# Optimization experiments

Measured on AMD Instinct MI355X. Metric: run time of the kernel, lower is better.

Reference implementation:

```python
import jax, jax.numpy as jnp
import numpy as np

N_NODES = 50000
N_EDGES = 640000
IN_DIM = 5
HID = 128
NUM_GRAPHS = 512


def _graph_conv(x, src, dst, W_rel, b_rel, W_root):
    # PyG GraphConv (aggr='add'): out = lin_rel(sum_{j in N(i)} x_j) + lin_root(x_i)
    agg = jax.ops.segment_sum(x[src], dst, num_segments=N_NODES)  # [N, d_in]
    return agg @ W_rel + b_rel + x @ W_root


def setup_inputs() -> dict:
    key = jax.random.key(0)
    ks = jax.random.split(key, 16)
    x = jax.random.normal(ks[0], (N_NODES, IN_DIM), dtype=jnp.float32)
    edge_index = jax.random.randint(ks[1], (2, N_EDGES), 0, N_NODES, dtype=jnp.int32)
    batch = jnp.sort(jax.random.randint(ks[2], (N_NODES,), 0, NUM_GRAPHS, dtype=jnp.int32))

    def lin_w(k, fan_in, fan_out):
        bound = 1.0 / np.sqrt(fan_in)
        return jax.random.uniform(k, (fan_in, fan_out), jnp.float32, -bound, bound)

    def lin_b(k, fan_in, fan_out):
        bound = 1.0 / np.sqrt(fan_in)
        return jax.random.uniform(k, (fan_out,), jnp.float32, -bound, bound)

    params = {}
    dims = [(IN_DIM, HID), (HID, HID), (HID, HID)]
    for i, (di, do) in enumerate(dims):
        params[f"W_rel{i}"] = lin_w(ks[3 + 3 * i], di, do)
        params[f"b_rel{i}"] = lin_b(ks[4 + 3 * i], di, do)
        params[f"W_root{i}"] = lin_w(ks[5 + 3 * i], di, do)
    params["W_lin"] = lin_w(ks[12], HID, 1)
    params["b_lin"] = lin_b(ks[13], HID, 1)
    return {"x": x, "edge_index": edge_index, "batch": batch, **params}


def reference(x, edge_index, batch,
              W_rel0, b_rel0, W_root0,
              W_rel1, b_rel1, W_root1,
              W_rel2, b_rel2, W_root2,
              W_lin, b_lin):
    src, dst = edge_index[0], edge_index[1]
    # convs[:-1] with ReLU
    h = jax.nn.relu(_graph_conv(x, src, dst, W_rel0, b_rel0, W_root0))
    h = jax.nn.relu(_graph_conv(h, src, dst, W_rel1, b_rel1, W_root1))
    # last conv, no activation
    h = _graph_conv(h, src, dst, W_rel2, b_rel2, W_root2)
    # global_mean_pool over batch ids
    sums = jax.ops.segment_sum(h, batch, num_segments=NUM_GRAPHS)  # [G, HID]
    cnts = jax.ops.segment_sum(jnp.ones((h.shape[0],), h.dtype), batch, num_segments=NUM_GRAPHS)
    pooled = sums / jnp.maximum(cnts, 1.0)[:, None]
    # dropout(p=0.01) is identity in eval mode
    logits = pooled @ W_lin + b_lin  # [G, 1]
    return jax.nn.sigmoid(logits)
```

## Files before the change

kernel.cpp:

```cpp
#include <hip/hip_runtime.h>
#include <hip/hip_bf16.h>
#include <math.h>

#define N_NODES 50000
#define N_EDGES 640000
#define IN_DIM 5
#define HID 128
#define NGRAPH 512
#define BUCKET 64
#define GEMM_NBLK ((N_NODES + 63) / 64)
#define EDGE_BLK (N_EDGES / 1024)
#define TPREP_BLK 32
#define NROW_BLK ((N_NODES + 255) / 256)

typedef unsigned short u16;
typedef __attribute__((ext_vector_type(8))) short bf16x8;
typedef __attribute__((ext_vector_type(8))) unsigned short u16x8;
typedef __attribute__((ext_vector_type(4))) float f32x4;
typedef __attribute__((ext_vector_type(8))) float f32x8;
typedef __attribute__((ext_vector_type(4), aligned(4))) float f32x4u;

__device__ __forceinline__ float bf2f(u16 u) {
  union { unsigned int i; float f; } v; v.i = ((unsigned int)u) << 16; return v.f;
}
__device__ __forceinline__ u16 f2bf(float f) {
  return __bfloat16_as_ushort(__float2bfloat16(f));
}

__global__ __launch_bounds__(256) void setup_k(const int* __restrict__ src,
                                               const int* __restrict__ dst,
                                               int* __restrict__ cnt,
                                               int* __restrict__ slot,
                                               const float* __restrict__ W1rel,
                                               const float* __restrict__ W1root,
                                               u16* __restrict__ T1rel, u16* __restrict__ T1root,
                                               const float* __restrict__ Wrel2,
                                               const float* __restrict__ Wroot2,
                                               const float* __restrict__ b2,
                                               const float* __restrict__ Wlin,
                                               float* __restrict__ wvecs,
                                               const int* __restrict__ batch,
                                               int* __restrict__ nrow) {
  int b = blockIdx.x;
  if (b < EDGE_BLK) {
    int e0 = (b * 256 + threadIdx.x) * 4;
    int4 s4 = *(const int4*)(src + e0);
    int4 d4 = *(const int4*)(dst + e0);
    int ss[4] = {s4.x, s4.y, s4.z, s4.w};
    int dd[4] = {d4.x, d4.y, d4.z, d4.w};
#pragma unroll
    for (int j = 0; j < 4; ++j) {
      int pos = atomicAdd(&cnt[dd[j]], 1);
      if (pos < BUCKET) slot[(size_t)dd[j] * BUCKET + pos] = ss[j];
    }
  } else if (b < EDGE_BLK + TPREP_BLK) {
    int idx4 = ((b - EDGE_BLK) * 256 + threadIdx.x) * 4;
    int which = idx4 >> 14;
    int i = idx4 & (HID * HID - 1);
    const float* W = which == 0 ? W1rel : W1root;
    u16* T = which == 0 ? T1rel : T1root;
    int k = i >> 7, n = i & 127;
    float4 w4 = *(const float4*)(W + i);
    T[(n + 0) * HID + k] = f2bf(w4.x);
    T[(n + 1) * HID + k] = f2bf(w4.y);
    T[(n + 2) * HID + k] = f2bf(w4.z);
    T[(n + 3) * HID + k] = f2bf(w4.w);
  } else if (b == EDGE_BLK + TPREP_BLK) {
    int t = threadIdx.x;
    if (t < 128) {
      float s = 0.f;
      for (int c = 0; c < HID; ++c) s = fmaf(Wrel2[t * HID + c], Wlin[c], s);
      wvecs[t] = s;
    } else {
      int k = t - 128;
      float s = 0.f;
      for (int c = 0; c < HID; ++c) s = fmaf(Wroot2[k * HID + c], Wlin[c], s);
      wvecs[128 + k] = s;
    }
    if (t == 0) {
      float s = 0.f;
      for (int c = 0; c < HID; ++c) s = fmaf(b2[c], Wlin[c], s);
      wvecs[256] = s;
    }
  } else {
    int n = (b - EDGE_BLK - TPREP_BLK - 1) * 256 + threadIdx.x;
    if (n < N_NODES) {
      int bg = batch[n];
      int bp = (n == 0) ? -1 : batch[n - 1];
      for (int g = bp + 1; g <= bg; ++g) nrow[g] = n;
      if (n == N_NODES - 1) {
        for (int g = bg + 1; g <= NGRAPH; ++g) nrow[g] = N_NODES;
      }
    }
  }
}

__global__ __launch_bounds__(256, 3) void proj_gemm_k(const float* __restrict__ x,
                                                      const int* __restrict__ cnt,
                                                      const int* __restrict__ slot,
                                                      const float* __restrict__ Wrel0,
                                                      const float* __restrict__ Wroot0,
                                                      const float* __restrict__ brel0,
                                                      const u16* __restrict__ WrelT,
                                                      const u16* __restrict__ WrootT,
                                                      const float* __restrict__ bias1,
                                                      u16* __restrict__ Z,
                                                      u16* __restrict__ R) {
  __shared__ u16 As[64][136];
  __shared__ float A5s[64][IN_DIM];
  const int tid = threadIdx.x;
  const int r0 = blockIdx.x * 64;

  {
    const int li = tid >> 2;
    const int l4 = tid & 3;
    const int node = r0 + li;
    float a[IN_DIM];
#pragma unroll
    for (int k = 0; k < IN_DIM; ++k) a[k] = 0.f;
    if (node < N_NODES) {
      int deg = min(cnt[node], BUCKET);
      size_t base = (size_t)node * BUCKET;
      for (int j = l4; j < deg; j += 4) {
        int s = slot[base + j];
        f32x4u xv = *(const f32x4u*)(x + (size_t)s * IN_DIM);
        float x4 = x[(size_t)s * IN_DIM + 4];
#pragma unroll
        for (int k = 0; k < 4; ++k) a[k] += xv[k];
        a[4] += x4;
      }
    }
#pragma unroll
    for (int k = 0; k < IN_DIM; ++k) {
      a[k] += __shfl_xor(a[k], 1, 64);
      a[k] += __shfl_xor(a[k], 2, 64);
    }
    if (l4 == 0) {
#pragma unroll
      for (int k = 0; k < IN_DIM; ++k) A5s[li][k] = a[k];
    }
  }
  __syncthreads();

  {
    const int c0 = (tid & 63) * 2;
    const int rg = tid >> 6;
    float wr0[IN_DIM], wr1[IN_DIM], wo0[IN_DIM], wo1[IN_DIM];
#pragma unroll
    for (int k = 0; k < IN_DIM; ++k) {
      wr0[k] = Wrel0[k * HID + c0];
      wr1[k] = Wrel0[k * HID + c0 + 1];
      wo0[k] = Wroot0[k * HID + c0];
      wo1[k] = Wroot0[k * HID + c0 + 1];
    }
    const float b0 = brel0[c0], b1 = brel0[c0 + 1];
#pragma unroll
    for (int i = 0; i < 16; ++i) {
      int row = rg * 16 + i;
      int grow = r0 + row;
      float v0 = 0.f, v1 = 0.f;
      if (grow < N_NODES) {
        v0 = b0; v1 = b1;
        f32x4u xv = *(const f32x4u*)(x + (size_t)grow * IN_DIM);
        float x4 = x[(size_t)grow * IN_DIM + 4];
        float xr[IN_DIM] = {xv[0], xv[1], xv[2], xv[3], x4};
#pragma unroll
        for (int k = 0; k < IN_DIM; ++k) {
          float a = A5s[row][k];
          v0 = fmaf(a, wr0[k], fmaf(xr[k], wo0[k], v0));
          v1 = fmaf(a, wr1[k], fmaf(xr[k], wo1[k], v1));
        }
      }
      ushort2 w2;
      w2.x = f2bf(fmaxf(v0, 0.f));
      w2.y = f2bf(fmaxf(v1, 0.f));
      *(ushort2*)&As[row][c0] = w2;
    }
  }
  __syncthreads();

  const int wv = tid >> 6, lane = tid & 63;
  const int m = lane & 15, quad = lane >> 4;
  const u16* WT = (wv < 2) ? WrelT : WrootT;
  const int n0 = (wv & 1) * 64;

  f32x4 acc[4][4];
#pragma unroll
  for (int mt = 0; mt < 4; ++mt)
#pragma unroll
    for (int nt = 0; nt < 4; ++nt) acc[mt][nt] = (f32x4){0.f, 0.f, 0.f, 0.f};

#pragma unroll
  for (int ks = 0; ks < 4; ++ks) {
    int kb = ks * 32;
    bf16x8 af[4], bf[4];
#pragma unroll
    for (int mt = 0; mt < 4; ++mt)
      af[mt] = *(const bf16x8*)&As[mt * 16 + m][kb + quad * 8];
#pragma unroll
    for (int nt = 0; nt < 4; ++nt)
      bf[nt] = *(const bf16x8*)(WT + (size_t)(n0 + nt * 16 + m) * HID + kb + quad * 8);
#pragma unroll
    for (int mt = 0; mt < 4; ++mt)
#pragma unroll
      for (int nt = 0; nt < 4; ++nt)
        acc[mt][nt] = __builtin_amdgcn_mfma_f32_16x16x32_bf16(af[mt], bf[nt], acc[mt][nt], 0, 0, 0);
  }

  if (wv < 2) {
#pragma unroll
    for (int mt = 0; mt < 4; ++mt)
#pragma unroll
      for (int nt = 0; nt < 4; ++nt) {
        int col = n0 + nt * 16 + m;
#pragma unroll
        for (int r = 0; r < 4; ++r) {
          int row = r0 + mt * 16 + quad * 4 + r;
          if (row < N_NODES) Z[(size_t)row * HID + col] = f2bf(acc[mt][nt][r]);
        }
      }
  } else {
    float bl[4];
#pragma unroll
    for (int nt = 0; nt < 4; ++nt) bl[nt] = bias1[n0 + nt * 16 + m];
#pragma unroll
    for (int mt = 0; mt < 4; ++mt)
#pragma unroll
      for (int nt = 0; nt < 4; ++nt) {
        int col = n0 + nt * 16 + m;
#pragma unroll
        for (int r = 0; r < 4; ++r) {
          int row = r0 + mt * 16 + quad * 4 + r;
          if (row < N_NODES) R[(size_t)row * HID + col] = f2bf(acc[mt][nt][r] + bl[nt]);
        }
      }
  }
}

__device__ __forceinline__ void gather_node(const u16* __restrict__ Z,
                                            const int* __restrict__ esrc,
                                            int beg, int end, int q, int f8,
                                            f32x8& out) {
  f32x8 a0, a1;
#pragma unroll
  for (int j = 0; j < 8; ++j) { a0[j] = 0.f; a1[j] = 0.f; }
  int e = beg + q;
  for (; e + 4 < end; e += 8) {
    int s0 = esrc[e];
    int s1 = esrc[e + 4];
    u16x8 za = *(const u16x8*)(Z + (size_t)s0 * HID + f8);
    u16x8 zb = *(const u16x8*)(Z + (size_t)s1 * HID + f8);
#pragma unroll
    for (int j = 0; j < 8; ++j) { a0[j] += bf2f(za[j]); a1[j] += bf2f(zb[j]); }
  }
  if (e < end) {
    int s0 = esrc[e];
    u16x8 za = *(const u16x8*)(Z + (size_t)s0 * HID + f8);
#pragma unroll
    for (int j = 0; j < 8; ++j) a0[j] += bf2f(za[j]);
  }
#pragma unroll
  for (int j = 0; j < 8; ++j) out[j] = a0[j] + a1[j];
}

__global__ __launch_bounds__(256) void agg_s_k(const u16* __restrict__ Z,
                                               const int* __restrict__ cnt,
                                               const int* __restrict__ slot,
                                               const u16* __restrict__ R,
                                               const float* __restrict__ wvecs,
                                               float* __restrict__ s_rel,
                                               float* __restrict__ s_root) {
  int wave = threadIdx.x >> 6;
  int lane = threadIdx.x & 63;
  int node = blockIdx.x * 4 + wave;
  if (node >= N_NODES) return;
  int q = lane >> 4;
  int l16 = lane & 15;
  int f8 = l16 * 8;
  int beg = node * BUCKET;
  int end = beg + min(cnt[node], BUCKET);
  f32x8 acc;
  gather_node(Z, slot, beg, end, q, f8, acc);
#pragma unroll
  for (int j = 0; j < 8; ++j) {
    acc[j] += __shfl_xor(acc[j], 16, 64);
    acc[j] += __shfl_xor(acc[j], 32, 64);
  }
  if (q == 0) {
    const u16* rp = R + (size_t)node * HID + f8;
    u16x8 r8 = *(const u16x8*)rp;
    float sr = 0.f, so = 0.f;
#pragma unroll
    for (int j = 0; j < 8; ++j) {
      float h = fmaxf(bf2f(r8[j]) + acc[j], 0.f);
      sr = fmaf(h, wvecs[f8 + j], sr);
      so = fmaf(h, wvecs[128 + f8 + j], so);
    }
#pragma unroll
    for (int w = 1; w < 16; w <<= 1) {
      sr += __shfl_xor(sr, w, 16);
      so += __shfl_xor(so, w, 16);
    }
    if (l16 == 0) {
      s_rel[node] = sr;
      s_root[node] = so;
    }
  }
}

__global__ __launch_bounds__(256) void pool_final_k(const float* __restrict__ s_rel,
                                                    const float* __restrict__ s_root,
                                                    const int* __restrict__ cnt,
                                                    const int* __restrict__ slot,
                                                    const int* __restrict__ nrow,
                                                    const float* __restrict__ wvecs,
                                                    const float* __restrict__ blin,
                                                    float* __restrict__ out) {
  int g = blockIdx.x;
  int n0 = nrow[g], n1 = nrow[g + 1];
  int wave = threadIdx.x >> 6;
  int lane = threadIdx.x & 63;
  float s = 0.f;
  for (int n = n0 + wave; n < n1; n += 4) {
    int deg = min(cnt[n], BUCKET);
    if (lane < deg) s += s_rel[slot[(size_t)n * BUCKET + lane]];
  }
  for (int n = n0 + threadIdx.x; n < n1; n += 256) s += s_root[n];
  __shared__ float red[4];
#pragma unroll
  for (int w = 32; w; w >>= 1) s += __shfl_down(s, w, 64);
  if (lane == 0) red[wave] = s;
  __syncthreads();
  if (threadIdx.x == 0) {
    float t = red[0] + red[1] + red[2] + red[3];
    float cntf = (float)(n1 - n0);
    float cmax = fmaxf(cntf, 1.f);
    float logit = (t + cntf * wvecs[256]) / cmax + blin[0];
    out[g] = 1.f / (1.f + expf(-logit));
  }
}


extern "C" void kernel_launch(void* const* d_in, const int* in_sizes, int n_in,
                              void* d_out, int out_size, void* d_ws, size_t ws_size,
                              hipStream_t stream) {
  const float* x      = (const float*)d_in[0];
  const int*   ei     = (const int*)d_in[1];
  const int*   batch  = (const int*)d_in[2];
  const float* Wrel0  = (const float*)d_in[3];
  const float* brel0  = (const float*)d_in[4];
  const float* Wroot0 = (const float*)d_in[5];
  const float* Wrel1  = (const float*)d_in[6];
  const float* brel1  = (const float*)d_in[7];
  const float* Wroot1 = (const float*)d_in[8];
  const float* Wrel2  = (const float*)d_in[9];
  const float* brel2  = (const float*)d_in[10];
  const float* Wroot2 = (const float*)d_in[11];
  const float* Wlin   = (const float*)d_in[12];
  const float* blin   = (const float*)d_in[13];
  float* out = (float*)d_out;
  const int* srcp = ei;
  const int* dstp = ei + N_EDGES;

  char* ws = (char*)d_ws;
  size_t off = 0;
  auto alloc = [&](size_t b) { size_t o = off; off += (b + 255) & ~(size_t)255; return (void*)(ws + o); };
  u16*  Z      = (u16*)alloc(sizeof(u16) * N_NODES * HID);
  u16*  R      = (u16*)alloc(sizeof(u16) * N_NODES * HID);
  float* s_rel  = (float*)alloc(sizeof(float) * N_NODES);
  float* s_root = (float*)alloc(sizeof(float) * N_NODES);
  u16* WT1rel  = (u16*)alloc(sizeof(u16) * HID * HID);
  u16* WT1root = (u16*)alloc(sizeof(u16) * HID * HID);
  float* wvecs = (float*)alloc(sizeof(float) * 260);
  int* nrow    = (int*)alloc(sizeof(int) * (NGRAPH + 1));
  int* slot    = (int*)alloc(sizeof(int) * (size_t)N_NODES * BUCKET);
  size_t zero_base = off;
  int*   cnt  = (int*)alloc(sizeof(int) * N_NODES);
  size_t zero_len = off - zero_base;

  hipMemsetAsync(ws + zero_base, 0, zero_len, stream);

  setup_k<<<EDGE_BLK + TPREP_BLK + 1 + NROW_BLK, 256, 0, stream>>>(
      srcp, dstp, cnt, slot, Wrel1, Wroot1, WT1rel, WT1root,
      Wrel2, Wroot2, brel2, Wlin, wvecs, batch, nrow);
  proj_gemm_k<<<GEMM_NBLK, 256, 0, stream>>>(x, cnt, slot, Wrel0, Wroot0, brel0,
                                             WT1rel, WT1root, brel1, Z, R);
  agg_s_k<<<(N_NODES + 3) / 4, 256, 0, stream>>>(Z, cnt, slot, R, wvecs, s_rel, s_root);
  pool_final_k<<<NGRAPH, 256, 0, stream>>>(s_rel, s_root, cnt, slot, nrow, wvecs, blin, out);
}
```

Measured before the change: 203.1 us.

## Replace per-node atomic bucket fill with two-pass binned CSR build using 16-bit sources

The fixed 64-slot per-node bucket is replaced by a two-pass binning sort. The first pass groups edges into 512-node bins with shared-memory histograms and one global atomic per bin. The second pass builds compact per-node segments inside each bin and stores source ids as 16-bit values. This removes per-edge global atomics on a 50000-entry counter and the large sparse slot array, and it halves index bandwidth in the gather kernels. In exchange it adds an extra kernel launch and two block-wide scans, and it relies on node ids fitting in 16 bits and on bins not exceeding their capacity.

Measured after the change: 203.1 us. No clear change (+0.0%).

```diff
diff --git a/kernel.cpp b/kernel.cpp
--- a/kernel.cpp
+++ b/kernel.cpp
@@ -7,11 +7,14 @@
 #define IN_DIM 5
 #define HID 128
 #define NGRAPH 512
-#define BUCKET 64
 #define GEMM_NBLK ((N_NODES + 63) / 64)
 #define EDGE_BLK (N_EDGES / 1024)
 #define TPREP_BLK 32
 #define NROW_BLK ((N_NODES + 255) / 256)
+#define NBIN 128
+#define BIN_SHIFT 9
+#define NBIN_ACTIVE ((N_NODES + 511) >> 9)
+#define BINCAP 8192
 
 typedef unsigned short u16;
 typedef __attribute__((ext_vector_type(8))) short bf16x8;
@@ -27,34 +30,72 @@
   return __bfloat16_as_ushort(__float2bfloat16(f));
 }
 
-__global__ __launch_bounds__(256) void setup_k(const int* __restrict__ src,
-                                               const int* __restrict__ dst,
-                                               int* __restrict__ cnt,
-                                               int* __restrict__ slot,
-                                               const float* __restrict__ W1rel,
-                                               const float* __restrict__ W1root,
-                                               u16* __restrict__ T1rel, u16* __restrict__ T1root,
-                                               const float* __restrict__ Wrel2,
-                                               const float* __restrict__ Wroot2,
-                                               const float* __restrict__ b2,
-                                               const float* __restrict__ Wlin,
-                                               float* __restrict__ wvecs,
-                                               const int* __restrict__ batch,
-                                               int* __restrict__ nrow) {
+__global__ __launch_bounds__(256) void binA_k(const int* __restrict__ src,
+                                              const int* __restrict__ dst,
+                                              int* __restrict__ bin_tail,
+                                              unsigned int* __restrict__ binned,
+                                              const float* __restrict__ W1rel,
+                                              const float* __restrict__ W1root,
+                                              u16* __restrict__ T1rel, u16* __restrict__ T1root,
+                                              const float* __restrict__ Wrel2,
+                                              const float* __restrict__ Wroot2,
+                                              const float* __restrict__ b2,
+                                              const float* __restrict__ Wlin,
+                                              float* __restrict__ wvecs,
+                                              const int* __restrict__ batch,
+                                              int* __restrict__ nrow) {
   int b = blockIdx.x;
+  int t = threadIdx.x;
   if (b < EDGE_BLK) {
-    int e0 = (b * 256 + threadIdx.x) * 4;
+    __shared__ int hist[NBIN];
+    __shared__ int scan_s[NBIN];
+    __shared__ int gbase[NBIN];
+    __shared__ int sc[256];
+    __shared__ unsigned int stage[1024];
+    __shared__ unsigned char binof[1024];
+    for (int i = t; i < NBIN; i += 256) hist[i] = 0;
+    __syncthreads();
+    int e0 = (b * 256 + t) * 4;
     int4 s4 = *(const int4*)(src + e0);
     int4 d4 = *(const int4*)(dst + e0);
     int ss[4] = {s4.x, s4.y, s4.z, s4.w};
     int dd[4] = {d4.x, d4.y, d4.z, d4.w};
+    int mybin[4], myoff[4];
 #pragma unroll
     for (int j = 0; j < 4; ++j) {
-      int pos = atomicAdd(&cnt[dd[j]], 1);
-      if (pos < BUCKET) slot[(size_t)dd[j] * BUCKET + pos] = ss[j];
+      mybin[j] = dd[j] >> BIN_SHIFT;
+      myoff[j] = atomicAdd(&hist[mybin[j]], 1);
+    }
+    __syncthreads();
+    int c = (t < NBIN) ? hist[t] : 0;
+    sc[t] = c;
+    __syncthreads();
+#pragma unroll
+    for (int o = 1; o < 256; o <<= 1) {
+      int u = (t >= o) ? sc[t - o] : 0;
+      __syncthreads();
+      sc[t] += u;
+      __syncthreads();
+    }
+    if (t < NBIN) {
+      scan_s[t] = sc[t] - c;
+      gbase[t] = (c > 0) ? atomicAdd(&bin_tail[t], c) : 0;
+    }
+    __syncthreads();
+#pragma unroll
+    for (int j = 0; j < 4; ++j) {
+      int pos = scan_s[mybin[j]] + myoff[j];
+      stage[pos] = ((unsigned int)dd[j] << 16) | (unsigned int)ss[j];
+      binof[pos] = (unsigned char)mybin[j];
+    }
+    __syncthreads();
+    for (int i = t; i < 1024; i += 256) {
+      int bb = binof[i];
+      int pos = gbase[bb] + (i - scan_s[bb]);
+      if (pos < BINCAP) binned[(size_t)bb * BINCAP + pos] = stage[i];
     }
   } else if (b < EDGE_BLK + TPREP_BLK) {
-    int idx4 = ((b - EDGE_BLK) * 256 + threadIdx.x) * 4;
+    int idx4 = ((b - EDGE_BLK) * 256 + t) * 4;
     int which = idx4 >> 14;
     int i = idx4 & (HID * HID - 1);
     const float* W = which == 0 ? W1rel : W1root;
@@ -66,7 +107,6 @@
     T[(n + 2) * HID + k] = f2bf(w4.z);
     T[(n + 3) * HID + k] = f2bf(w4.w);
   } else if (b == EDGE_BLK + TPREP_BLK) {
-    int t = threadIdx.x;
     if (t < 128) {
       float s = 0.f;
       for (int c = 0; c < HID; ++c) s = fmaf(Wrel2[t * HID + c], Wlin[c], s);
@@ -83,7 +123,7 @@
       wvecs[256] = s;
     }
   } else {
-    int n = (b - EDGE_BLK - TPREP_BLK - 1) * 256 + threadIdx.x;
+    int n = (b - EDGE_BLK - TPREP_BLK - 1) * 256 + t;
     if (n < N_NODES) {
       int bg = batch[n];
       int bp = (n == 0) ? -1 : batch[n - 1];
@@ -95,9 +135,74 @@
   }
 }
 
+__global__ __launch_bounds__(256) void binB_k(const int* __restrict__ bin_tail,
+                                              const unsigned int* __restrict__ binned,
+                                              u16* __restrict__ esrc2,
+                                              int* __restrict__ row_start,
+                                              int* __restrict__ cnt2) {
+  __shared__ int hist[512];
+  __shared__ int sc[256];
+  __shared__ int off_s[512];
+  __shared__ int total0_s;
+  int b = blockIdx.x;
+  int t = threadIdx.x;
+  int ecnt = min(bin_tail[b], BINCAP);
+  size_t base = (size_t)b * BINCAP;
+  for (int i = t; i < 512; i += 256) hist[i] = 0;
+  __syncthreads();
+  for (int e = t; e < ecnt; e += 256) {
+    int d = binned[base + e] >> 16;
+    atomicAdd(&hist[d & 511], 1);
+  }
+  __syncthreads();
+  int excl0, excl1, tot0;
+  {
+    int c = hist[t];
+    sc[t] = c; __syncthreads();
+#pragma unroll
+    for (int o = 1; o < 256; o <<= 1) {
+      int u = (t >= o) ? sc[t - o] : 0; __syncthreads();
+      sc[t] += u; __syncthreads();
+    }
+    excl0 = sc[t] - c;
+    if (t == 255) total0_s = sc[255];
+    __syncthreads();
+    tot0 = total0_s;
+    __syncthreads();
+  }
+  {
+    int c = hist[256 + t];
+    sc[t] = c; __syncthreads();
+#pragma unroll
+    for (int o = 1; o < 256; o <<= 1) {
+      int u = (t >= o) ? sc[t - o] : 0; __syncthreads();
+      sc[t] += u; __syncthreads();
+    }
+    excl1 = sc[t] - c + tot0;
+  }
+  __syncthreads();
+  int n0 = b << BIN_SHIFT;
+  off_s[t] = excl0;
+  off_s[256 + t] = excl1;
+  {
+    int n = n0 + t;
+    if (n < N_NODES) { row_start[n] = (int)base + excl0; cnt2[n] = hist[t]; }
+    n = n0 + 256 + t;
+    if (n < N_NODES) { row_start[n] = (int)base + excl1; cnt2[n] = hist[256 + t]; }
+  }
+  __syncthreads();
+  for (int e = t; e < ecnt; e += 256) {
+    unsigned int rec = binned[base + e];
+    int d = (rec >> 16) & 511;
+    int pos = atomicAdd(&off_s[d], 1);
+    esrc2[base + pos] = (u16)(rec & 0xFFFFu);
+  }
+}
+
 __global__ __launch_bounds__(256, 3) void proj_gemm_k(const float* __restrict__ x,
-                                                      const int* __restrict__ cnt,
-                                                      const int* __restrict__ slot,
+                                                      const int* __restrict__ row_start,
+                                                      const int* __restrict__ cnt2,
+                                                      const u16* __restrict__ esrc2,
                                                       const float* __restrict__ Wrel0,
                                                       const float* __restrict__ Wroot0,
                                                       const float* __restrict__ brel0,
@@ -119,10 +224,10 @@
 #pragma unroll
     for (int k = 0; k < IN_DIM; ++k) a[k] = 0.f;
     if (node < N_NODES) {
-      int deg = min(cnt[node], BUCKET);
-      size_t base = (size_t)node * BUCKET;
-      for (int j = l4; j < deg; j += 4) {
-        int s = slot[base + j];
+      int beg = row_start[node];
+      int cn = cnt2[node];
+      for (int j = l4; j < cn; j += 4) {
+        int s = esrc2[beg + j];
         f32x4u xv = *(const f32x4u*)(x + (size_t)s * IN_DIM);
         float x4 = x[(size_t)s * IN_DIM + 4];
 #pragma unroll
@@ -238,7 +343,7 @@
 }
 
 __device__ __forceinline__ void gather_node(const u16* __restrict__ Z,
-                                            const int* __restrict__ esrc,
+                                            const u16* __restrict__ esrc,
                                             int beg, int end, int q, int f8,
                                             f32x8& out) {
   f32x8 a0, a1;
@@ -264,8 +369,9 @@
 }
 
 __global__ __launch_bounds__(256) void agg_s_k(const u16* __restrict__ Z,
-                                               const int* __restrict__ cnt,
-                                               const int* __restrict__ slot,
+                                               const int* __restrict__ row_start,
+                                               const int* __restrict__ cnt2,
+                                               const u16* __restrict__ esrc2,
                                                const u16* __restrict__ R,
                                                const float* __restrict__ wvecs,
                                                float* __restrict__ s_rel,
@@ -277,10 +383,10 @@
   int q = lane >> 4;
   int l16 = lane & 15;
   int f8 = l16 * 8;
-  int beg = node * BUCKET;
-  int end = beg + min(cnt[node], BUCKET);
+  int beg = row_start[node];
+  int end = beg + cnt2[node];
   f32x8 acc;
-  gather_node(Z, slot, beg, end, q, f8, acc);
+  gather_node(Z, esrc2, beg, end, q, f8, acc);
 #pragma unroll
   for (int j = 0; j < 8; ++j) {
     acc[j] += __shfl_xor(acc[j], 16, 64);
@@ -310,8 +416,9 @@
 
 __global__ __launch_bounds__(256) void pool_final_k(const float* __restrict__ s_rel,
                                                     const float* __restrict__ s_root,
-                                                    const int* __restrict__ cnt,
-                                                    const int* __restrict__ slot,
+                                                    const int* __restrict__ row_start,
+                                                    const int* __restrict__ cnt2,
+                                                    const u16* __restrict__ esrc2,
                                                     const int* __restrict__ nrow,
                                                     const float* __restrict__ wvecs,
                                                     const float* __restrict__ blin,
@@ -322,8 +429,8 @@
   int lane = threadIdx.x & 63;
   float s = 0.f;
   for (int n = n0 + wave; n < n1; n += 4) {
-    int deg = min(cnt[n], BUCKET);
-    if (lane < deg) s += s_rel[slot[(size_t)n * BUCKET + lane]];
+    int c = min(cnt2[n], 64);
+    if (lane < c) s += s_rel[esrc2[row_start[n] + lane]];
   }
   for (int n = n0 + threadIdx.x; n < n1; n += 256) s += s_root[n];
   __shared__ float red[4];
@@ -373,18 +480,25 @@
   u16* WT1root = (u16*)alloc(sizeof(u16) * HID * HID);
   float* wvecs = (float*)alloc(sizeof(float) * 260);
   int* nrow    = (int*)alloc(sizeof(int) * (NGRAPH + 1));
-  int* slot    = (int*)alloc(sizeof(int) * (size_t)N_NODES * BUCKET);
+  unsigned int* binned = (unsigned int*)alloc(sizeof(unsigned int) * (size_t)NBIN * BINCAP);
+  u16* esrc2   = (u16*)alloc(sizeof(u16) * (size_t)NBIN * BINCAP);
+  int* row_start = (int*)alloc(sizeof(int) * N_NODES);
+  int* cnt2      = (int*)alloc(sizeof(int) * N_NODES);
   size_t zero_base = off;
-  int*   cnt  = (int*)alloc(sizeof(int) * N_NODES);
+  int* bin_tail = (int*)alloc(sizeof(int) * NBIN);
   size_t zero_len = off - zero_base;
 
   hipMemsetAsync(ws + zero_base, 0, zero_len, stream);
 
-  setup_k<<<EDGE_BLK + TPREP_BLK + 1 + NROW_BLK, 256, 0, stream>>>(
-      srcp, dstp, cnt, slot, Wrel1, Wroot1, WT1rel, WT1root,
+  binA_k<<<EDGE_BLK + TPREP_BLK + 1 + NROW_BLK, 256, 0, stream>>>(
+      srcp, dstp, bin_tail, binned, Wrel1, Wroot1, WT1rel, WT1root,
       Wrel2, Wroot2, brel2, Wlin, wvecs, batch, nrow);
-  proj_gemm_k<<<GEMM_NBLK, 256, 0, stream>>>(x, cnt, slot, Wrel0, Wroot0, brel0,
+  binB_k<<<NBIN_ACTIVE, 256, 0, stream>>>(bin_tail, binned, esrc2, row_start, cnt2);
+  proj_gemm_k<<<GEMM_NBLK, 256, 0, stream>>>(x, row_start, cnt2, esrc2,
+                                             Wrel0, Wroot0, brel0,
                                              WT1rel, WT1root, brel1, Z, R);
-  agg_s_k<<<(N_NODES + 3) / 4, 256, 0, stream>>>(Z, cnt, slot, R, wvecs, s_rel, s_root);
-  pool_final_k<<<NGRAPH, 256, 0, stream>>>(s_rel, s_root, cnt, slot, nrow, wvecs, blin, out);
-}
+  agg_s_k<<<(N_NODES + 3) / 4, 256, 0, stream>>>(Z, row_start, cnt2, esrc2, R, wvecs,
+                                                 s_rel, s_root);
+  pool_final_k<<<NGRAPH, 256, 0, stream>>>(s_rel, s_root, row_start, cnt2, esrc2,
+                                           nrow, wvecs, blin, out);
+}
```
